# Performance work log

Hardware: AMD Instinct MI355X
Metric: run time of the kernel (lower is better)

Reference implementation:

```python
import jax, jax.numpy as jnp
from jax import lax
import numpy as np

B, N = 8, 8192
NPOINT, RADIUS, NSAMPLE = 2048, 0.4, 64
EPS = 1e-5


def setup_inputs() -> dict:
    key = jax.random.key(0)
    ks = jax.random.split(key, 8)
    d = {
        'xyz': jax.random.normal(ks[0], (B, N, 3), jnp.float32),
        'features': jax.random.normal(ks[1], (B, 64, N), jnp.float32),
        'W0': jax.random.normal(ks[2], (64, 67), jnp.float32) * 0.1,
        'g0': jnp.ones((64,), jnp.float32), 'b0': jnp.zeros((64,), jnp.float32),
        'm0': jnp.zeros((64,), jnp.float32), 'v0': jnp.ones((64,), jnp.float32),
        'W1': jax.random.normal(ks[3], (64, 64), jnp.float32) * 0.1,
        'g1': jnp.ones((64,), jnp.float32), 'b1': jnp.zeros((64,), jnp.float32),
        'm1': jnp.zeros((64,), jnp.float32), 'v1': jnp.ones((64,), jnp.float32),
        'W2': jax.random.normal(ks[4], (128, 64), jnp.float32) * 0.1,
        'g2': jnp.ones((128,), jnp.float32), 'b2': jnp.zeros((128,), jnp.float32),
        'm2': jnp.zeros((128,), jnp.float32), 'v2': jnp.ones((128,), jnp.float32),
    }
    return d


def fps(xyz, npoint):
    # sequential furthest point sampling, start at index 0 (as in CUDA op)
    b = xyz.shape[0]
    first = jnp.zeros((b,), jnp.int32)
    d0 = jnp.sum((xyz - xyz[:, :1]) ** 2, -1)  # (B,N) dist to point 0

    def body(dist, _):
        nxt = jnp.argmax(dist, -1).astype(jnp.int32)
        p = jnp.take_along_axis(xyz, nxt[:, None, None].astype(jnp.int32), axis=1)
        dist = jnp.minimum(dist, jnp.sum((xyz - p) ** 2, -1))
        return dist, nxt

    _, rest = lax.scan(body, d0, None, length=npoint - 1)  # rest: (npoint-1, B)
    return jnp.concatenate([first[:, None], rest.T], axis=1)  # (B, npoint)


def ball_query(xyz, new_xyz, radius, nsample):
    # (B,P,N) squared distances
    d2 = jnp.sum((new_xyz[:, :, None, :] - xyz[:, None, :, :]) ** 2, -1)
    mask = d2 < radius * radius
    # stable sort: in-radius indices first, in original order (matches CUDA fill order)
    order = jnp.argsort(jnp.where(mask, 0, 1).astype(jnp.int32), axis=-1, stable=True)
    idx = order[..., :nsample]
    cnt = jnp.sum(mask, -1)  # (B,P)
    pos = jnp.arange(nsample)
    return jnp.where(pos < cnt[..., None], idx, idx[..., :1])  # pad with first found


def group(x, idx):
    # x (B,N,D), idx (B,P,S) -> (B,P,S,D)
    return jnp.take_along_axis(x[:, None], idx[..., None], axis=2)


def reference(xyz, features, W0, g0, b0, m0, v0, W1, g1, b1, m1, v1, W2, g2, b2, m2, v2):
    inds = fps(xyz, NPOINT)                                   # (B,P)
    new_xyz = jnp.take_along_axis(xyz, inds[..., None], axis=1)  # (B,P,3)
    idx = ball_query(xyz, new_xyz, RADIUS, NSAMPLE)           # (B,P,S)
    gxyz = group(xyz, idx) - new_xyz[:, :, None, :]           # (B,P,S,3) centered
    gfeat = group(jnp.swapaxes(features, 1, 2), idx)          # (B,P,S,C)
    x = jnp.concatenate([gxyz, gfeat], -1)                    # use_xyz concat
    x = jnp.transpose(x, (0, 3, 1, 2))                        # (B,C+3,P,S)
    for W, g, b, m, v in ((W0, g0, b0, m0, v0), (W1, g1, b1, m1, v1), (W2, g2, b2, m2, v2)):
        x = jnp.einsum('oi,bips->bops', W, x)                 # 1x1 conv
        scale = g / jnp.sqrt(v + EPS)
        x = (x - m[:, None, None]) * scale[:, None, None] + b[:, None, None]
        x = jax.nn.relu(x)
    new_features = jnp.max(x, -1)                             # max pool over nsample -> (B,128,P)
    return new_xyz, new_features, inds
```

## Files before the change

kernel.cpp:

```cpp
#include <hip/hip_runtime.h>
#include <cstdint>
#include <cstddef>

#define BATCH   8
#define NPTS    8192
#define NPOINT  2048
#define NSAMPLE 64
#define K0      67
#define C2      128

typedef float v2f __attribute__((ext_vector_type(2)));

__device__ __forceinline__ float d2e(float ax, float ay, float az,
                                     float bx, float by, float bz) {
#pragma clang fp contract(off)
  float dx = ax - bx;
  float dy = ay - by;
  float dz = az - bz;
  float t0 = dx * dx;
  float t1 = dy * dy;
  float t2 = dz * dz;
  return (t0 + t1) + t2;
}

__device__ __forceinline__ float dpp_max_f32(float x) {
  int v;
  v = __builtin_amdgcn_update_dpp(__float_as_int(x), __float_as_int(x), 0xB1, 0xF, 0xF, false);
  x = fmaxf(x, __int_as_float(v));
  v = __builtin_amdgcn_update_dpp(__float_as_int(x), __float_as_int(x), 0x4E, 0xF, 0xF, false);
  x = fmaxf(x, __int_as_float(v));
  v = __builtin_amdgcn_update_dpp(__float_as_int(x), __float_as_int(x), 0x141, 0xF, 0xF, false);
  x = fmaxf(x, __int_as_float(v));
  v = __builtin_amdgcn_update_dpp(__float_as_int(x), __float_as_int(x), 0x140, 0xF, 0xF, false);
  x = fmaxf(x, __int_as_float(v));
  v = __builtin_amdgcn_update_dpp(__float_as_int(x), __float_as_int(x), 0x142, 0xA, 0xF, false);
  x = fmaxf(x, __int_as_float(v));
  v = __builtin_amdgcn_update_dpp(__float_as_int(x), __float_as_int(x), 0x143, 0xC, 0xF, false);
  x = fmaxf(x, __int_as_float(v));
  return __int_as_float(__builtin_amdgcn_readlane(__float_as_int(x), 63));
}

__device__ __forceinline__ int dpp_min_i32(int x) {
  int v;
  v = __builtin_amdgcn_update_dpp(x, x, 0xB1, 0xF, 0xF, false); x = min(x, v);
  v = __builtin_amdgcn_update_dpp(x, x, 0x4E, 0xF, 0xF, false); x = min(x, v);
  v = __builtin_amdgcn_update_dpp(x, x, 0x141, 0xF, 0xF, false); x = min(x, v);
  v = __builtin_amdgcn_update_dpp(x, x, 0x140, 0xF, 0xF, false); x = min(x, v);
  v = __builtin_amdgcn_update_dpp(x, x, 0x142, 0xA, 0xF, false); x = min(x, v);
  v = __builtin_amdgcn_update_dpp(x, x, 0x143, 0xC, 0xF, false); x = min(x, v);
  return __builtin_amdgcn_readlane(x, 63);
}

__global__ __launch_bounds__(512) void fps_kernel(const float* __restrict__ xyz,
                                                  float* __restrict__ out_xyz,
                                                  float* __restrict__ out_inds) {
  const int b = blockIdx.x;
  const int tid = threadIdx.x;
  const int lane = tid & 63, w = tid >> 6;

  __shared__ float2 sxy[NPTS];
  __shared__ float  szl[NPTS];
  __shared__ unsigned short sslot[NPOINT];
  __shared__ unsigned long long wred[2][8] __attribute__((aligned(16)));

  const float* xb = xyz + (size_t)b * NPTS * 3;

  for (int k = 0; k < 16; k++) {
    int i = tid + k * 512;
    sxy[i] = make_float2(xb[i * 3 + 0], xb[i * 3 + 1]);
    szl[i] = xb[i * 3 + 2];
  }
  __syncthreads();

  const float2 q0xy = sxy[0];
  const float q0x = q0xy.x, q0y = q0xy.y, q0z = szl[0];

  const int base = tid * 16;
  v2f px2[8], py2[8], pz2[8], dd2[8];
  {
#pragma clang fp contract(off)
#pragma unroll
    for (int k = 0; k < 8; k++) {
      float2 a = sxy[base + 2 * k];
      float2 c = sxy[base + 2 * k + 1];
      px2[k] = (v2f){a.x, c.x};
      py2[k] = (v2f){a.y, c.y};
      pz2[k] = (v2f){szl[base + 2 * k], szl[base + 2 * k + 1]};
      v2f dx = px2[k] - q0x;
      v2f dy = py2[k] - q0y;
      v2f dz = pz2[k] - q0z;
      v2f t0 = dx * dx;
      v2f t1 = dy * dy;
      v2f t2 = dz * dz;
      dd2[k] = (t0 + t1) + t2;
    }
  }
  if (tid == 0) sslot[0] = 0;

  {
    float bv = -1.f; int bj = base;
#pragma unroll
    for (int k = 0; k < 8; k++) {
      float d0 = dd2[k].x, d1 = dd2[k].y;
      bool c0 = d0 > bv; bv = c0 ? d0 : bv; bj = c0 ? base + 2 * k : bj;
      bool c1 = d1 > bv; bv = c1 ? d1 : bv; bj = c1 ? base + 2 * k + 1 : bj;
    }
    float vm = dpp_max_f32(bv);
    int ci = (bv == vm) ? bj : 0x7FFFFFFF;
    int widx = dpp_min_i32(ci);
    if (lane == 0)
      wred[0][w] = ((unsigned long long)(~__float_as_uint(vm)) << 32) | (unsigned)widx;
  }
  __syncthreads();

  for (int t = 1; t < NPOINT; ++t) {
    const ulonglong2* wv = (const ulonglong2*)wred[(t - 1) & 1];
    ulonglong2 p0 = wv[0], p1 = wv[1], p2 = wv[2], p3 = wv[3];
    unsigned long long g0 = (p0.y < p0.x) ? p0.y : p0.x;
    unsigned long long g1 = (p1.y < p1.x) ? p1.y : p1.x;
    unsigned long long g2 = (p2.y < p2.x) ? p2.y : p2.x;
    unsigned long long g3 = (p3.y < p3.x) ? p3.y : p3.x;
    g0 = (g1 < g0) ? g1 : g0; g2 = (g3 < g2) ? g3 : g2;
    g0 = (g2 < g0) ? g2 : g0;
    const int nxt = (int)(g0 & 0xFFFFFFFFu);
    const float2 qxy = sxy[nxt];
    const float qx = qxy.x, qy = qxy.y, qz = szl[nxt];
    if (tid == 0) sslot[t] = (unsigned short)nxt;

    float bv = -1.f; int bj = base;
    {
#pragma clang fp contract(off)
#pragma unroll
      for (int k = 0; k < 8; k++) {
        v2f dx = px2[k] - qx;
        v2f dy = py2[k] - qy;
        v2f dz = pz2[k] - qz;
        v2f t0 = dx * dx;
        v2f t1 = dy * dy;
        v2f t2 = dz * dz;
        v2f d = (t0 + t1) + t2;
        v2f nd;
        nd.x = fminf(dd2[k].x, d.x);
        nd.y = fminf(dd2[k].y, d.y);
        dd2[k] = nd;
        bool c0 = nd.x > bv; bv = c0 ? nd.x : bv; bj = c0 ? base + 2 * k : bj;
        bool c1 = nd.y > bv; bv = c1 ? nd.y : bv; bj = c1 ? base + 2 * k + 1 : bj;
      }
    }
    float vm = dpp_max_f32(bv);
    int ci = (bv == vm) ? bj : 0x7FFFFFFF;
    int widx = dpp_min_i32(ci);
    if (lane == 0)
      wred[t & 1][w] = ((unsigned long long)(~__float_as_uint(vm)) << 32) | (unsigned)widx;
    __syncthreads();
  }

  for (int t = tid; t < NPOINT; t += 512) {
    int o = (int)sslot[t];
    float2 xy = sxy[o];
    out_inds[b * NPOINT + t] = (float)o;
    out_xyz[((size_t)b * NPOINT + t) * 3 + 0] = xy.x;
    out_xyz[((size_t)b * NPOINT + t) * 3 + 1] = xy.y;
    out_xyz[((size_t)b * NPOINT + t) * 3 + 2] = szl[o];
  }
}

__global__ __launch_bounds__(128) void prep_kernel(
    const float* __restrict__ W0, const float* __restrict__ g0,
    const float* __restrict__ b0, const float* __restrict__ m0,
    const float* __restrict__ v0, const float* __restrict__ g1,
    const float* __restrict__ b1, const float* __restrict__ m1,
    const float* __restrict__ v1, const float* __restrict__ g2,
    const float* __restrict__ b2, const float* __restrict__ m2,
    const float* __restrict__ v2, float* __restrict__ wsp) {
  const int tid = threadIdx.x;
  if (tid < 64) {
    float s0 = g0[tid] / sqrtf(v0[tid] + 1e-5f);
    wsp[4 * tid + 0] = s0 * W0[tid * K0 + 0];
    wsp[4 * tid + 1] = s0 * W0[tid * K0 + 1];
    wsp[4 * tid + 2] = s0 * W0[tid * K0 + 2];
    wsp[4 * tid + 3] = b0[tid] - m0[tid] * s0;
    wsp[640 + tid] = s0;
    float s1 = g1[tid] / sqrtf(v1[tid] + 1e-5f);
    wsp[256 + tid] = s1; wsp[320 + tid] = b1[tid] - m1[tid] * s1;
  }
  float s2 = g2[tid] / sqrtf(v2[tid] + 1e-5f);
  wsp[384 + tid] = s2; wsp[512 + tid] = b2[tid] - m2[tid] * s2;
}

__global__ __launch_bounds__(256) void zfeat_kernel(const float* __restrict__ xyz,
                                                    const float* __restrict__ feat,
                                                    const float* __restrict__ W0,
                                                    const float* __restrict__ wsp,
                                                    float* __restrict__ szp) {
  __shared__ float ftile[64][64];
  __shared__ float sxyz[192];
  const int bt = blockIdx.x;
  const int b = bt >> 7, nt = bt & 127;
  const int tid = threadIdx.x;
  const int lane = tid & 63, w = tid >> 6;

  const float* fb = feat + (size_t)b * 64 * NPTS + (size_t)nt * 64;
#pragma unroll
  for (int r = w; r < 64; r += 4)
    ftile[r][lane] = fb[(size_t)r * NPTS + lane];
  if (tid < 192)
    sxyz[tid] = xyz[((size_t)b * NPTS + (size_t)nt * 64) * 3 + tid];

  float w0x = W0[lane * K0 + 0], w0y = W0[lane * K0 + 1], w0z = W0[lane * K0 + 2];
  float wf[64];
#pragma unroll
  for (int i = 0; i < 64; i++) wf[i] = W0[lane * K0 + 3 + i];
  const float s0 = wsp[640 + lane];
  __syncthreads();

  float* ob = szp + ((size_t)b * NPTS + (size_t)nt * 64) * 64;
  for (int u = w; u < 64; u += 4) {
    float acc = w0x * sxyz[u * 3 + 0] + w0y * sxyz[u * 3 + 1] + w0z * sxyz[u * 3 + 2];
#pragma unroll
    for (int i = 0; i < 64; i++) acc = fmaf(wf[i], ftile[i][u], acc);
    ob[(size_t)u * 64 + lane] = acc * s0;
  }
}

__global__ __launch_bounds__(256) void ballq_kernel(const float* __restrict__ xyz,
                                                    const float* __restrict__ new_xyz,
                                                    int* __restrict__ ball) {
  const int lane = threadIdx.x & 63;
  const int q = blockIdx.x * 4 + (threadIdx.x >> 6);
  const int b = q >> 11;
  const float RR = (float)(0.4 * 0.4);
  const float cx = new_xyz[(size_t)q * 3 + 0];
  const float cy = new_xyz[(size_t)q * 3 + 1];
  const float cz = new_xyz[(size_t)q * 3 + 2];
  const float* xb = xyz + (size_t)b * NPTS * 3;
  int cnt = 0, firsti = -1;
  for (int base = 0; base < NPTS; base += 64) {
    int i = base + lane;
    float xx = xb[i * 3 + 0], yy = xb[i * 3 + 1], zz = xb[i * 3 + 2];
    float d2 = d2e(xx, yy, zz, cx, cy, cz);
    bool m = d2 < RR;
    unsigned long long mask = __ballot(m);
    if (mask) {
      if (firsti < 0) firsti = base + (__ffsll((unsigned long long)mask) - 1);
      int pos = cnt + (int)__popcll(mask & ((1ull << lane) - 1ull));
      if (m && pos < NSAMPLE) ball[(size_t)q * NSAMPLE + pos] = i;
      cnt += (int)__popcll(mask);
      if (cnt >= NSAMPLE) break;
    }
  }
  for (int s = cnt + lane; s < NSAMPLE; s += 64)
    ball[(size_t)q * NSAMPLE + s] = firsti;
}

#define QPW 4
__global__ __launch_bounds__(256, 2) void mlp_kernel(
    const float* __restrict__ szp, const int* __restrict__ ball,
    const float* __restrict__ new_xyz, const float* __restrict__ W1,
    const float* __restrict__ W2, const float* __restrict__ wsp,
    float* __restrict__ out_feat) {
  __shared__ float ylds[4][64];
  __shared__ int   blds[4][64];
  const int tid = threadIdx.x;
  const int lane = tid & 63, wid = tid >> 6;

  float4 w1v[16], w2av[16], w2bv[16];
  const float4* W1r = (const float4*)(W1 + lane * 64);
  const float4* W2ar = (const float4*)(W2 + lane * 64);
  const float4* W2br = (const float4*)(W2 + (lane + 64) * 64);
#pragma unroll
  for (int i = 0; i < 16; i++) { w1v[i] = W1r[i]; w2av[i] = W2ar[i]; w2bv[i] = W2br[i]; }
  const float4 A = ((const float4*)wsp)[lane];
  const float sc1l = wsp[256 + lane], sh1l = wsp[320 + lane];
  const float sc2al = wsp[384 + lane], sh2al = wsp[512 + lane];
  const float sc2bl = wsp[448 + lane], sh2bl = wsp[576 + lane];

  for (int qi = 0; qi < QPW; qi++) {
    const int q = blockIdx.x * (4 * QPW) + qi * 4 + wid;
    const int b = q >> 11, p = q & 2047;

    const float cx = new_xyz[(size_t)q * 3 + 0];
    const float cy = new_xyz[(size_t)q * 3 + 1];
    const float cz = new_xyz[(size_t)q * 3 + 2];
    const float hc = A.w - (A.x * cx + A.y * cy + A.z * cz);

    blds[wid][lane] = ball[(size_t)q * NSAMPLE + lane];
    const float* szb = szp + (size_t)b * NPTS * 64;
    __builtin_amdgcn_s_waitcnt(0);

    float vA = 0.f, vB = 0.f;
    int idx0 = blds[wid][0];
    float fcur = szb[(size_t)idx0 * 64 + lane];
    const float4* yv = (const float4*)ylds[wid];

    for (int s = 0; s < NSAMPLE; s++) {
      int sn = (s < NSAMPLE - 1) ? s + 1 : s;
      int idxn = blds[wid][sn];
      float fnext = szb[(size_t)idxn * 64 + lane];

      float y0 = fmaxf(fcur + hc, 0.f);
      ylds[wid][lane] = y0;
      float a0 = 0.f, a1 = 0.f, a2 = 0.f, a3 = 0.f;
#pragma unroll
      for (int i = 0; i < 16; i++) {
        float4 y = yv[i];
        a0 = fmaf(w1v[i].x, y.x, a0);
        a1 = fmaf(w1v[i].y, y.y, a1);
        a2 = fmaf(w1v[i].z, y.z, a2);
        a3 = fmaf(w1v[i].w, y.w, a3);
      }
      float y1 = fmaxf(fmaf((a0 + a1) + (a2 + a3), sc1l, sh1l), 0.f);
      ylds[wid][lane] = y1;
      float c0 = 0.f, c1 = 0.f, c2 = 0.f, c3 = 0.f;
      float e0 = 0.f, e1 = 0.f, e2 = 0.f, e3 = 0.f;
#pragma unroll
      for (int i = 0; i < 16; i++) {
        float4 y = yv[i];
        c0 = fmaf(w2av[i].x, y.x, c0);
        c1 = fmaf(w2av[i].y, y.y, c1);
        c2 = fmaf(w2av[i].z, y.z, c2);
        c3 = fmaf(w2av[i].w, y.w, c3);
        e0 = fmaf(w2bv[i].x, y.x, e0);
        e1 = fmaf(w2bv[i].y, y.y, e1);
        e2 = fmaf(w2bv[i].z, y.z, e2);
        e3 = fmaf(w2bv[i].w, y.w, e3);
      }
      float y2a = fmaxf(fmaf((c0 + c1) + (c2 + c3), sc2al, sh2al), 0.f);
      float y2b = fmaxf(fmaf((e0 + e1) + (e2 + e3), sc2bl, sh2bl), 0.f);
      vA = fmaxf(vA, y2a);
      vB = fmaxf(vB, y2b);
      fcur = fnext;
    }
    out_feat[((size_t)b * C2 + lane) * NPOINT + p] = vA;
    out_feat[((size_t)b * C2 + lane + 64) * NPOINT + p] = vB;
  }
}

extern "C" void kernel_launch(void* const* d_in, const int* in_sizes, int n_in,
                              void* d_out, int out_size, void* d_ws, size_t ws_size,
                              hipStream_t stream) {
  const float* xyz  = (const float*)d_in[0];
  const float* feat = (const float*)d_in[1];
  const float* W0 = (const float*)d_in[2];
  const float* g0 = (const float*)d_in[3];
  const float* b0 = (const float*)d_in[4];
  const float* m0 = (const float*)d_in[5];
  const float* v0 = (const float*)d_in[6];
  const float* W1 = (const float*)d_in[7];
  const float* g1 = (const float*)d_in[8];
  const float* b1 = (const float*)d_in[9];
  const float* m1 = (const float*)d_in[10];
  const float* v1 = (const float*)d_in[11];
  const float* W2 = (const float*)d_in[12];
  const float* g2 = (const float*)d_in[13];
  const float* b2 = (const float*)d_in[14];
  const float* m2 = (const float*)d_in[15];
  const float* v2 = (const float*)d_in[16];

  float* out = (float*)d_out;
  float* out_xyz  = out;
  float* out_feat = out + 49152;
  float* out_inds = out + 49152 + 2097152;

  int*   ball = (int*)d_ws;
  float* szp  = (float*)((char*)d_ws + 4194304);
  float* wsp  = (float*)((char*)d_ws + 20971520);

  hipLaunchKernelGGL(prep_kernel, dim3(1), dim3(128), 0, stream,
                     W0, g0, b0, m0, v0, g1, b1, m1, v1, g2, b2, m2, v2, wsp);
  hipLaunchKernelGGL(zfeat_kernel, dim3(BATCH * (NPTS / 64)), dim3(256), 0, stream,
                     xyz, feat, W0, wsp, szp);
  hipLaunchKernelGGL(fps_kernel, dim3(BATCH), dim3(512), 0, stream,
                     xyz, out_xyz, out_inds);
  hipLaunchKernelGGL(ballq_kernel, dim3((BATCH * NPOINT) / 4), dim3(256), 0, stream,
                     xyz, out_xyz, ball);
  hipLaunchKernelGGL(mlp_kernel, dim3((BATCH * NPOINT) / (4 * QPW)), dim3(256), 0, stream,
                     szp, ball, out_xyz, W1, W2, wsp, out_feat);
}
```

Before: 2.555 ms.

## Fuse ball query into MLP kernel and pack FPS argmax into single key reduction

Ball query moves inside mlp_kernel, so each wave finds its neighbour indices directly into LDS. This removes the separate ballq launch and the global round-trip of the index buffer. The FPS per-wave argmax now packs the inverted distance and the 13-bit index into one 64-bit key and runs a single DPP min reduction instead of a max followed by an index-min. This shortens the sequential critical path per iteration. The risk is that the fused ball-query scan's latency now sits inside the register-heavy MLP kernel with lower occupancy.

After: 2.646 ms. 1.04x slower.

```diff
diff --git a/kernel.cpp b/kernel.cpp
--- a/kernel.cpp
+++ b/kernel.cpp
@@ -23,32 +23,26 @@
   return (t0 + t1) + t2;
 }
 
-__device__ __forceinline__ float dpp_max_f32(float x) {
-  int v;
-  v = __builtin_amdgcn_update_dpp(__float_as_int(x), __float_as_int(x), 0xB1, 0xF, 0xF, false);
-  x = fmaxf(x, __int_as_float(v));
-  v = __builtin_amdgcn_update_dpp(__float_as_int(x), __float_as_int(x), 0x4E, 0xF, 0xF, false);
-  x = fmaxf(x, __int_as_float(v));
-  v = __builtin_amdgcn_update_dpp(__float_as_int(x), __float_as_int(x), 0x141, 0xF, 0xF, false);
-  x = fmaxf(x, __int_as_float(v));
-  v = __builtin_amdgcn_update_dpp(__float_as_int(x), __float_as_int(x), 0x140, 0xF, 0xF, false);
-  x = fmaxf(x, __int_as_float(v));
-  v = __builtin_amdgcn_update_dpp(__float_as_int(x), __float_as_int(x), 0x142, 0xA, 0xF, false);
-  x = fmaxf(x, __int_as_float(v));
-  v = __builtin_amdgcn_update_dpp(__float_as_int(x), __float_as_int(x), 0x143, 0xC, 0xF, false);
-  x = fmaxf(x, __int_as_float(v));
-  return __int_as_float(__builtin_amdgcn_readlane(__float_as_int(x), 63));
-}
-
-__device__ __forceinline__ int dpp_min_i32(int x) {
-  int v;
-  v = __builtin_amdgcn_update_dpp(x, x, 0xB1, 0xF, 0xF, false); x = min(x, v);
-  v = __builtin_amdgcn_update_dpp(x, x, 0x4E, 0xF, 0xF, false); x = min(x, v);
-  v = __builtin_amdgcn_update_dpp(x, x, 0x141, 0xF, 0xF, false); x = min(x, v);
-  v = __builtin_amdgcn_update_dpp(x, x, 0x140, 0xF, 0xF, false); x = min(x, v);
-  v = __builtin_amdgcn_update_dpp(x, x, 0x142, 0xA, 0xF, false); x = min(x, v);
-  v = __builtin_amdgcn_update_dpp(x, x, 0x143, 0xC, 0xF, false); x = min(x, v);
-  return __builtin_amdgcn_readlane(x, 63);
+__device__ __forceinline__ unsigned long long dpp_min_key(unsigned long long k) {
+#define KSTEP(CTRL, RM, BM)                                                    \
+  {                                                                            \
+    int lo = (int)k, hi = (int)(k >> 32);                                      \
+    int lo2 = __builtin_amdgcn_update_dpp(lo, lo, CTRL, RM, BM, false);        \
+    int hi2 = __builtin_amdgcn_update_dpp(hi, hi, CTRL, RM, BM, false);        \
+    unsigned long long k2 =                                                    \
+        ((unsigned long long)(unsigned)hi2 << 32) | (unsigned)lo2;             \
+    k = (k2 < k) ? k2 : k;                                                     \
+  }
+  KSTEP(0xB1, 0xF, 0xF)
+  KSTEP(0x4E, 0xF, 0xF)
+  KSTEP(0x141, 0xF, 0xF)
+  KSTEP(0x140, 0xF, 0xF)
+  KSTEP(0x142, 0xA, 0xF)
+  KSTEP(0x143, 0xC, 0xF)
+#undef KSTEP
+  int lo = __builtin_amdgcn_readlane((int)k, 63);
+  int hi = __builtin_amdgcn_readlane((int)(k >> 32), 63);
+  return ((unsigned long long)(unsigned)hi << 32) | (unsigned)lo;
 }
 
 __global__ __launch_bounds__(512) void fps_kernel(const float* __restrict__ xyz,
@@ -105,11 +99,10 @@
       bool c0 = d0 > bv; bv = c0 ? d0 : bv; bj = c0 ? base + 2 * k : bj;
       bool c1 = d1 > bv; bv = c1 ? d1 : bv; bj = c1 ? base + 2 * k + 1 : bj;
     }
-    float vm = dpp_max_f32(bv);
-    int ci = (bv == vm) ? bj : 0x7FFFFFFF;
-    int widx = dpp_min_i32(ci);
-    if (lane == 0)
-      wred[0][w] = ((unsigned long long)(~__float_as_uint(vm)) << 32) | (unsigned)widx;
+    unsigned long long kk =
+        ((unsigned long long)(~__float_as_uint(bv)) << 13) | (unsigned)bj;
+    kk = dpp_min_key(kk);
+    if (lane == 0) wred[0][w] = kk;
   }
   __syncthreads();
 
@@ -122,7 +115,7 @@
     unsigned long long g3 = (p3.y < p3.x) ? p3.y : p3.x;
     g0 = (g1 < g0) ? g1 : g0; g2 = (g3 < g2) ? g3 : g2;
     g0 = (g2 < g0) ? g2 : g0;
-    const int nxt = (int)(g0 & 0xFFFFFFFFu);
+    const int nxt = (int)(g0 & 0x1FFFu);
     const float2 qxy = sxy[nxt];
     const float qx = qxy.x, qy = qxy.y, qz = szl[nxt];
     if (tid == 0) sslot[t] = (unsigned short)nxt;
@@ -147,11 +140,10 @@
         bool c1 = nd.y > bv; bv = c1 ? nd.y : bv; bj = c1 ? base + 2 * k + 1 : bj;
       }
     }
-    float vm = dpp_max_f32(bv);
-    int ci = (bv == vm) ? bj : 0x7FFFFFFF;
-    int widx = dpp_min_i32(ci);
-    if (lane == 0)
-      wred[t & 1][w] = ((unsigned long long)(~__float_as_uint(vm)) << 32) | (unsigned)widx;
+    unsigned long long kk =
+        ((unsigned long long)(~__float_as_uint(bv)) << 13) | (unsigned)bj;
+    kk = dpp_min_key(kk);
+    if (lane == 0) wred[t & 1][w] = kk;
     __syncthreads();
   }
 
@@ -223,39 +215,9 @@
   }
 }
 
-__global__ __launch_bounds__(256) void ballq_kernel(const float* __restrict__ xyz,
-                                                    const float* __restrict__ new_xyz,
-                                                    int* __restrict__ ball) {
-  const int lane = threadIdx.x & 63;
-  const int q = blockIdx.x * 4 + (threadIdx.x >> 6);
-  const int b = q >> 11;
-  const float RR = (float)(0.4 * 0.4);
-  const float cx = new_xyz[(size_t)q * 3 + 0];
-  const float cy = new_xyz[(size_t)q * 3 + 1];
-  const float cz = new_xyz[(size_t)q * 3 + 2];
-  const float* xb = xyz + (size_t)b * NPTS * 3;
-  int cnt = 0, firsti = -1;
-  for (int base = 0; base < NPTS; base += 64) {
-    int i = base + lane;
-    float xx = xb[i * 3 + 0], yy = xb[i * 3 + 1], zz = xb[i * 3 + 2];
-    float d2 = d2e(xx, yy, zz, cx, cy, cz);
-    bool m = d2 < RR;
-    unsigned long long mask = __ballot(m);
-    if (mask) {
-      if (firsti < 0) firsti = base + (__ffsll((unsigned long long)mask) - 1);
-      int pos = cnt + (int)__popcll(mask & ((1ull << lane) - 1ull));
-      if (m && pos < NSAMPLE) ball[(size_t)q * NSAMPLE + pos] = i;
-      cnt += (int)__popcll(mask);
-      if (cnt >= NSAMPLE) break;
-    }
-  }
-  for (int s = cnt + lane; s < NSAMPLE; s += 64)
-    ball[(size_t)q * NSAMPLE + s] = firsti;
-}
-
 #define QPW 4
 __global__ __launch_bounds__(256, 2) void mlp_kernel(
-    const float* __restrict__ szp, const int* __restrict__ ball,
+    const float* __restrict__ xyz, const float* __restrict__ szp,
     const float* __restrict__ new_xyz, const float* __restrict__ W1,
     const float* __restrict__ W2, const float* __restrict__ wsp,
     float* __restrict__ out_feat) {
@@ -274,28 +236,47 @@
   const float sc1l = wsp[256 + lane], sh1l = wsp[320 + lane];
   const float sc2al = wsp[384 + lane], sh2al = wsp[512 + lane];
   const float sc2bl = wsp[448 + lane], sh2bl = wsp[576 + lane];
+  const float RR = (float)(0.4 * 0.4);
+
+  int* bl = blds[wid];
+  const float4* yv = (const float4*)ylds[wid];
 
   for (int qi = 0; qi < QPW; qi++) {
     const int q = blockIdx.x * (4 * QPW) + qi * 4 + wid;
     const int b = q >> 11, p = q & 2047;
+    const float* xb = xyz + (size_t)b * NPTS * 3;
+    const float* szb = szp + (size_t)b * NPTS * 64;
 
     const float cx = new_xyz[(size_t)q * 3 + 0];
     const float cy = new_xyz[(size_t)q * 3 + 1];
     const float cz = new_xyz[(size_t)q * 3 + 2];
     const float hc = A.w - (A.x * cx + A.y * cy + A.z * cz);
 
-    blds[wid][lane] = ball[(size_t)q * NSAMPLE + lane];
-    const float* szb = szp + (size_t)b * NPTS * 64;
+    int cnt = 0, firsti = -1;
+    for (int base2 = 0; base2 < NPTS; base2 += 64) {
+      int i = base2 + lane;
+      float xx = xb[i * 3 + 0], yy = xb[i * 3 + 1], zz = xb[i * 3 + 2];
+      float dq = d2e(xx, yy, zz, cx, cy, cz);
+      bool m = dq < RR;
+      unsigned long long mask = __ballot(m);
+      if (mask) {
+        if (firsti < 0) firsti = base2 + (__ffsll((unsigned long long)mask) - 1);
+        int pos = cnt + (int)__popcll(mask & ((1ull << lane) - 1ull));
+        if (m && pos < NSAMPLE) bl[pos] = i;
+        cnt += (int)__popcll(mask);
+        if (cnt >= NSAMPLE) break;
+      }
+    }
+    for (int s = cnt + lane; s < NSAMPLE; s += 64) bl[s] = firsti;
     __builtin_amdgcn_s_waitcnt(0);
 
     float vA = 0.f, vB = 0.f;
-    int idx0 = blds[wid][0];
+    int idx0 = bl[0];
     float fcur = szb[(size_t)idx0 * 64 + lane];
-    const float4* yv = (const float4*)ylds[wid];
 
     for (int s = 0; s < NSAMPLE; s++) {
       int sn = (s < NSAMPLE - 1) ? s + 1 : s;
-      int idxn = blds[wid][sn];
+      int idxn = bl[sn];
       float fnext = szb[(size_t)idxn * 64 + lane];
 
       float y0 = fmaxf(fcur + hc, 0.f);
@@ -362,7 +343,6 @@
   float* out_feat = out + 49152;
   float* out_inds = out + 49152 + 2097152;
 
-  int*   ball = (int*)d_ws;
   float* szp  = (float*)((char*)d_ws + 4194304);
   float* wsp  = (float*)((char*)d_ws + 20971520);
 
@@ -372,8 +352,6 @@
                      xyz, feat, W0, wsp, szp);
   hipLaunchKernelGGL(fps_kernel, dim3(BATCH), dim3(512), 0, stream,
                      xyz, out_xyz, out_inds);
-  hipLaunchKernelGGL(ballq_kernel, dim3((BATCH * NPOINT) / 4), dim3(256), 0, stream,
-                     xyz, out_xyz, ball);
   hipLaunchKernelGGL(mlp_kernel, dim3((BATCH * NPOINT) / (4 * QPW)), dim3(256), 0, stream,
-                     szp, ball, out_xyz, W1, W2, wsp, out_feat);
-}
+                     xyz, szp, out_xyz, W1, W2, wsp, out_feat);
+}
```
